# Kernel optimization log

Hardware: AMD Instinct MI355X
Metric: run time of the kernel (lower is better)

The kernel has to match this reference:

```python
import jax, jax.numpy as jnp
import numpy as np

B = 512
D_MODEL = 512
D_STATE = 128
D_CONV = 2
EXPAND = 2
D_INNER = EXPAND * D_MODEL          # 1024
DT_RANK = (D_MODEL + 15) // 16      # 32 (mamba default 'auto')
HIDDEN = 256


def setup_inputs() -> dict:
    key = jax.random.key(0)
    ks = jax.random.split(key, 12)
    s = 0.02
    f32 = jnp.float32
    inp = {
        "x": jax.random.normal(ks[0], (B, D_MODEL), f32),
        # Mamba params (torch Linear weight layout: [out, in])
        "in_proj_w": jax.random.normal(ks[1], (2 * D_INNER, D_MODEL), f32) * s,
        "conv_w": jax.random.normal(ks[2], (D_INNER, D_CONV), f32) * s,  # depthwise kernel
        "conv_b": jnp.zeros((D_INNER,), f32),
        "x_proj_w": jax.random.normal(ks[3], (DT_RANK + 2 * D_STATE, D_INNER), f32) * s,
        "dt_proj_w": jax.random.normal(ks[4], (D_INNER, DT_RANK), f32) * s,
        "dt_proj_b": jax.random.normal(ks[5], (D_INNER,), f32) * s,
        "A_log": jnp.log(jnp.broadcast_to(
            jnp.arange(1, D_STATE + 1, dtype=f32), (D_INNER, D_STATE)).copy()),
        "D": jnp.ones((D_INNER,), f32),
        "out_proj_w": jax.random.normal(ks[6], (D_MODEL, D_INNER), f32) * s,
        # head params
        "fc1_w": jax.random.normal(ks[7], (HIDDEN, D_MODEL), f32) * s,
        "fc1_b": jnp.zeros((HIDDEN,), f32),
        "fc5_w": jax.random.normal(ks[8], (1, HIDDEN), f32) * s,
        "fc5_b": jnp.zeros((1,), f32),
    }
    return inp


def _mamba(x3, in_proj_w, conv_w, conv_b, x_proj_w, dt_proj_w, dt_proj_b,
           A_log, D, out_proj_w):
    # x3: [B, L, d_model]
    Bn, L, _ = x3.shape
    xz = jnp.einsum('bld,ed->ble', x3, in_proj_w)          # [B, L, 2*d_inner]
    xin, z = xz[..., :D_INNER], xz[..., D_INNER:]
    # depthwise causal conv1d (kernel D_CONV, padding D_CONV-1, truncated to L)
    xp = jnp.pad(xin, ((0, 0), (D_CONV - 1, 0), (0, 0)))
    conv = conv_b
    for k in range(D_CONV):
        conv = conv + conv_w[:, k] * xp[:, k:k + L, :]
    xin = jax.nn.silu(conv)                                 # [B, L, d_inner]
    x_dbl = jnp.einsum('blc,ec->ble', xin, x_proj_w)        # [B, L, dt_rank+2*d_state]
    dt = x_dbl[..., :DT_RANK]
    Bm = x_dbl[..., DT_RANK:DT_RANK + D_STATE]              # [B, L, d_state]
    Cm = x_dbl[..., DT_RANK + D_STATE:]                     # [B, L, d_state]
    dt = jax.nn.softplus(jnp.einsum('blr,cr->blc', dt, dt_proj_w) + dt_proj_b)
    A = -jnp.exp(A_log)                                     # [d_inner, d_state]
    dA = jnp.exp(dt[..., None] * A)                         # [B, L, d_inner, d_state]
    dBu = dt[..., None] * Bm[:, :, None, :] * xin[..., None]

    def step(h, t):
        dA_t, dBu_t, C_t = t
        h = dA_t * h + dBu_t                                # [B, d_inner, d_state]
        y_t = jnp.einsum('bcs,bs->bc', h, C_t)
        return h, y_t

    h0 = jnp.zeros((Bn, D_INNER, D_STATE), x3.dtype)
    _, ys = jax.lax.scan(step, h0, (dA.transpose(1, 0, 2, 3),
                                    dBu.transpose(1, 0, 2, 3),
                                    Cm.transpose(1, 0, 2)))
    y = ys.transpose(1, 0, 2)                               # [B, L, d_inner]
    y = (y + D * xin) * jax.nn.silu(z)
    return jnp.einsum('blc,dc->bld', y, out_proj_w)         # [B, L, d_model]


def reference(x, in_proj_w, conv_w, conv_b, x_proj_w, dt_proj_w, dt_proj_b,
              A_log, D, out_proj_w, fc1_w, fc1_b, fc5_w, fc5_b):
    h = _mamba(x[:, None, :], in_proj_w, conv_w, conv_b, x_proj_w,
               dt_proj_w, dt_proj_b, A_log, D, out_proj_w)[:, 0, :]
    h = h @ fc1_w.T + fc1_b
    h = jnp.where(h >= 0, h, 0.1 * h)   # LeakyReLU(0.1); dropout is eval-mode identity
    h = h @ fc5_w.T + fc5_b
    return jax.nn.sigmoid(h)            # [B, 1]
```

## Files before the change

kernel.cpp:

```cpp
#include <hip/hip_runtime.h>
#include <hip/hip_bf16.h>
#include <cstddef>

typedef __attribute__((ext_vector_type(8))) short short8;
typedef __attribute__((ext_vector_type(4))) float f32x4;

#define MFMA16(a, b, c) __builtin_amdgcn_mfma_f32_16x16x32_bf16((a), (b), (c), 0, 0, 0)

static __device__ __forceinline__ unsigned short f2bf(float f) {
    unsigned int u = __float_as_uint(f);
    u = (u + 0x7FFFu + ((u >> 16) & 1u)) >> 16;
    return (unsigned short)u;
}
static __device__ __forceinline__ float bf2f(unsigned short h) {
    return __uint_as_float(((unsigned int)h) << 16);
}
static __device__ __forceinline__ float silu_f(float v) { return v / (1.f + expf(-v)); }

static __device__ __forceinline__ short8 cvt_frag(const float* __restrict__ p) {
    float4 a = *reinterpret_cast<const float4*>(p);
    float4 b = *reinterpret_cast<const float4*>(p + 4);
    union { short8 s; unsigned int u[4]; } r;
    asm("v_cvt_pk_bf16_f32 %0, %1, %2" : "=v"(r.u[0]) : "v"(a.x), "v"(a.y));
    asm("v_cvt_pk_bf16_f32 %0, %1, %2" : "=v"(r.u[1]) : "v"(a.z), "v"(a.w));
    asm("v_cvt_pk_bf16_f32 %0, %1, %2" : "=v"(r.u[2]) : "v"(b.x), "v"(b.y));
    asm("v_cvt_pk_bf16_f32 %0, %1, %2" : "=v"(r.u[3]) : "v"(b.z), "v"(b.w));
    return r.s;
}

enum : size_t {
    O_X     = 0,
    O_WIP   = O_X    + 512 * 512,
    O_WXP   = O_WIP  + 2048 * 512,
    O_WDT   = O_WXP  + 288 * 1024,
    O_WOUT  = O_WDT  + 1024 * 32,
    O_WFC1  = O_WOUT + 512 * 1024,
    O_XIN   = O_WFC1 + 256 * 512,
    O_SZ    = O_XIN  + 512 * 1024,
    O_Y     = O_SZ   + 512 * 1024,
    O_F32   = O_Y    + 512 * 1024,
};
#define N_XDBLF (512 * 288)
#define N_MOUTF (512 * 512)
#define N_ZERO  (N_XDBLF + N_MOUTF)

static __device__ __forceinline__ void cvt_seg(const float* __restrict__ s,
                                               unsigned short* __restrict__ d,
                                               int n, int gt, int np)
{
    for (int i = gt * 4; i < n; i += np * 4) {
        float4 v = *reinterpret_cast<const float4*>(s + i);
        ushort4 o;
        o.x = f2bf(v.x); o.y = f2bf(v.y); o.z = f2bf(v.z); o.w = f2bf(v.w);
        *reinterpret_cast<ushort4*>(d + i) = o;
    }
}

__global__ __launch_bounds__(256) void k_convert(
    const float* __restrict__ x,    const float* __restrict__ wip,
    const float* __restrict__ wxp,  const float* __restrict__ wdt,
    const float* __restrict__ wout, const float* __restrict__ wfc1,
    unsigned short* __restrict__ wsb)
{
    const int gt = blockIdx.x * blockDim.x + threadIdx.x;
    const int np = gridDim.x * blockDim.x;
    cvt_seg(x,    wsb + O_X,    512 * 512,  gt, np);
    cvt_seg(wip,  wsb + O_WIP,  2048 * 512, gt, np);
    cvt_seg(wxp,  wsb + O_WXP,  288 * 1024, gt, np);
    cvt_seg(wdt,  wsb + O_WDT,  1024 * 32,  gt, np);
    cvt_seg(wout, wsb + O_WOUT, 512 * 1024, gt, np);
    cvt_seg(wfc1, wsb + O_WFC1, 256 * 512,  gt, np);
    float* z = (float*)(wsb + O_F32);
    const float4 z4 = make_float4(0.f, 0.f, 0.f, 0.f);
    for (int i = gt * 4; i < N_ZERO; i += np * 4)
        *reinterpret_cast<float4*>(z + i) = z4;
}

__global__ __launch_bounds__(256, 4) void k_s1(
    unsigned short* __restrict__ wsb,
    const float* __restrict__ cw, const float* __restrict__ cb)
{
    const int tid = threadIdx.x;
    const int w = tid >> 6, lane = tid & 63, l15 = lane & 15, g = lane >> 4;
    const int n0 = blockIdx.x * 64 + w * 16;
    const int m0 = blockIdx.y * 16;

    const unsigned short* arow = wsb + O_X   + (size_t)(m0 + l15) * 512 + g * 8;
    const unsigned short* brow = wsb + O_WIP + (size_t)(n0 + l15) * 512 + g * 8;

    f32x4 acc = {};
#pragma unroll 4
    for (int k0 = 0; k0 < 512; k0 += 32) {
        short8 a = *reinterpret_cast<const short8*>(arow + k0);
        short8 b = *reinterpret_cast<const short8*>(brow + k0);
        acc = MFMA16(a, b, acc);
    }
    const bool xhalf = (blockIdx.x < 16);
    unsigned short* dst = wsb + (xhalf ? O_XIN : O_SZ);
    int n = n0 + l15;
    int c = xhalf ? n : n - 1024;
    float cwv = 0.f, cbv = 0.f;
    if (xhalf) { cwv = cw[2 * n + 1]; cbv = cb[n]; }
#pragma unroll
    for (int i = 0; i < 4; ++i) {
        float v = acc[i];
        v = xhalf ? silu_f(cbv + cwv * v) : silu_f(v);
        dst[(size_t)(m0 + g * 4 + i) * 1024 + c] = f2bf(v);
    }
}

__global__ __launch_bounds__(256, 4) void k_s2(
    unsigned short* __restrict__ wsb, float* __restrict__ xdblf)
{
    const int tid = threadIdx.x;
    const int w = tid >> 6, lane = tid & 63, l15 = lane & 15, g = lane >> 4;
    const int n0 = blockIdx.x * 16;
    const int m0 = blockIdx.y * 64 + w * 16;
    const int kq = blockIdx.z * 256;

    const unsigned short* arow = wsb + O_XIN + (size_t)(m0 + l15) * 1024 + kq + g * 8;
    const unsigned short* brow = wsb + O_WXP + (size_t)(n0 + l15) * 1024 + kq + g * 8;

    f32x4 acc = {};
#pragma unroll 4
    for (int k0 = 0; k0 < 256; k0 += 32) {
        short8 a = *reinterpret_cast<const short8*>(arow + k0);
        short8 b = *reinterpret_cast<const short8*>(brow + k0);
        acc = MFMA16(a, b, acc);
    }
#pragma unroll
    for (int i = 0; i < 4; ++i)
        atomicAdd(&xdblf[(size_t)(m0 + g * 4 + i) * 288 + n0 + l15], acc[i]);
}

__global__ __launch_bounds__(256, 4) void k_s3(
    unsigned short* __restrict__ wsb, const float* __restrict__ xdblf,
    const float* __restrict__ dtb, const float* __restrict__ Dv)
{
    __shared__ float bcp[16][17];
    __shared__ float bc_s[16];
    const int tid = threadIdx.x;
    const int w = tid >> 6, lane = tid & 63, l15 = lane & 15, g = lane >> 4;
    const int n0 = blockIdx.x * 64;
    const int m0 = blockIdx.y * 16;

    {
        int r = tid >> 4, p = tid & 15;
        const float* row = xdblf + (size_t)(m0 + r) * 288;
        float s = 0.f;
#pragma unroll
        for (int q = 0; q < 8; ++q)
            s += row[32 + p * 8 + q] * row[160 + p * 8 + q];
        bcp[r][p] = s;
    }
    short8 a3 = cvt_frag(xdblf + (size_t)(m0 + l15) * 288 + g * 8);
    __syncthreads();
    if (tid < 16) {
        float s = 0.f;
#pragma unroll
        for (int p = 0; p < 16; ++p) s += bcp[tid][p];
        bc_s[tid] = s;
    }
    __syncthreads();

    const unsigned short* xinb = wsb + O_XIN;
    const unsigned short* szb  = wsb + O_SZ;
    unsigned short* yb = wsb + O_Y;
    const f32x4 z4 = {0.f, 0.f, 0.f, 0.f};
    int n = n0 + w * 16 + l15;
    short8 b = *reinterpret_cast<const short8*>(wsb + O_WDT + (size_t)n * 32 + g * 8);
    f32x4 acc = MFMA16(a3, b, z4);
    float dtbv = dtb[n], Dvv = Dv[n];
#pragma unroll
    for (int i = 0; i < 4; ++i) {
        int r = m0 + g * 4 + i;
        float dtv = acc[i] + dtbv;
        dtv = (dtv > 20.f) ? dtv : log1pf(expf(dtv));
        float yv = bf2f(xinb[(size_t)r * 1024 + n]) *
                   (dtv * bc_s[g * 4 + i] + Dvv) *
                   bf2f(szb[(size_t)r * 1024 + n]);
        yb[(size_t)r * 1024 + n] = f2bf(yv);
    }
}

__global__ __launch_bounds__(256, 4) void k_s4(
    unsigned short* __restrict__ wsb, float* __restrict__ moutf)
{
    const int tid = threadIdx.x;
    const int w = tid >> 6, lane = tid & 63, l15 = lane & 15, g = lane >> 4;
    const int n0 = blockIdx.x * 64 + w * 16;
    const int m0 = blockIdx.y * 16;
    const int kq = blockIdx.z * 512;

    const unsigned short* arow = wsb + O_Y    + (size_t)(m0 + l15) * 1024 + kq + g * 8;
    const unsigned short* brow = wsb + O_WOUT + (size_t)(n0 + l15) * 1024 + kq + g * 8;

    f32x4 acc = {};
#pragma unroll 4
    for (int k0 = 0; k0 < 512; k0 += 32) {
        short8 a = *reinterpret_cast<const short8*>(arow + k0);
        short8 b = *reinterpret_cast<const short8*>(brow + k0);
        acc = MFMA16(a, b, acc);
    }
#pragma unroll
    for (int i = 0; i < 4; ++i)
        atomicAdd(&moutf[(size_t)(m0 + g * 4 + i) * 512 + n0 + l15], acc[i]);
}

__global__ __launch_bounds__(512, 2) void k_s5(
    const float* __restrict__ moutf, unsigned short* __restrict__ wsb,
    const float* __restrict__ bfc1, const float* __restrict__ wfc5,
    const float* __restrict__ bfc5, float* __restrict__ out)
{
    __shared__ float red[16][8];
    const int tid = threadIdx.x;
    const int w = tid >> 6, lane = tid & 63, l15 = lane & 15, g = lane >> 4;
    const int m0 = blockIdx.x * 16;

    const float* arow = moutf + (size_t)(m0 + l15) * 512 + g * 8;
    const unsigned short* brow = wsb + O_WFC1 + (size_t)(w * 32 + l15) * 512 + g * 8;

    f32x4 acc[2] = {};
#pragma unroll 4
    for (int k0 = 0; k0 < 512; k0 += 32) {
        short8 a = cvt_frag(arow + k0);
#pragma unroll
        for (int f = 0; f < 2; ++f) {
            short8 b = *reinterpret_cast<const short8*>(brow + (size_t)f * 16 * 512 + k0);
            acc[f] = MFMA16(a, b, acc[f]);
        }
    }
    float part[4] = {0.f, 0.f, 0.f, 0.f};
#pragma unroll
    for (int f = 0; f < 2; ++f) {
        int n = w * 32 + f * 16 + l15;
        float b1 = bfc1[n], w5 = wfc5[n];
#pragma unroll
        for (int i = 0; i < 4; ++i) {
            float v = acc[f][i] + b1;
            v = v >= 0.f ? v : 0.1f * v;
            part[i] = fmaf(v, w5, part[i]);
        }
    }
#pragma unroll
    for (int off = 1; off < 16; off <<= 1)
#pragma unroll
        for (int i = 0; i < 4; ++i) part[i] += __shfl_xor(part[i], off, 64);
    if (l15 == 0)
#pragma unroll
        for (int i = 0; i < 4; ++i) red[g * 4 + i][w] = part[i];
    __syncthreads();
    if (tid < 16) {
        float s = 0.f;
#pragma unroll
        for (int j = 0; j < 8; ++j) s += red[tid][j];
        out[m0 + tid] = 1.f / (1.f + expf(-(s + bfc5[0])));
    }
}

extern "C" void kernel_launch(void* const* d_in, const int* in_sizes, int n_in,
                              void* d_out, int out_size, void* d_ws, size_t ws_size,
                              hipStream_t stream)
{
    const float* x    = (const float*)d_in[0];
    const float* wip  = (const float*)d_in[1];
    const float* cw   = (const float*)d_in[2];
    const float* cb   = (const float*)d_in[3];
    const float* wxp  = (const float*)d_in[4];
    const float* wdt  = (const float*)d_in[5];
    const float* bdt  = (const float*)d_in[6];
    const float* Dv   = (const float*)d_in[8];
    const float* wout = (const float*)d_in[9];
    const float* wfc1 = (const float*)d_in[10];
    const float* bfc1 = (const float*)d_in[11];
    const float* wfc5 = (const float*)d_in[12];
    const float* bfc5 = (const float*)d_in[13];
    float* out = (float*)d_out;

    unsigned short* wsb = (unsigned short*)d_ws;
    float* xdblf = (float*)(wsb + O_F32);
    float* moutf = xdblf + N_XDBLF;

    k_convert<<<dim3(1024),    256, 0, stream>>>(x, wip, wxp, wdt, wout, wfc1, wsb);
    k_s1     <<<dim3(32, 32),  256, 0, stream>>>(wsb, cw, cb);
    k_s2     <<<dim3(18, 8, 4),256, 0, stream>>>(wsb, xdblf);
    k_s3     <<<dim3(16, 32),  256, 0, stream>>>(wsb, xdblf, bdt, Dv);
    k_s4     <<<dim3(8, 32, 2),256, 0, stream>>>(wsb, moutf);
    k_s5     <<<dim3(32),      512, 0, stream>>>(moutf, wsb, bfc1, wfc5, bfc5, out);
}
```

Measured before the change: 142.2 us.

## Fold out_proj into fc1 weights and fuse final two GEMM stages

Uses associativity to precompute W45 = fc1_w @ out_proj_w (256x1024) inside the prep kernel via an LDS-transposed MFMA, then computes the head GEMM directly from y against W45. This removes the out_proj GEMM kernel, its atomicAdd reduction, the moutf zeroing, and one launch. The cost is an extra weight-product GEMM each call inside prep (256 of the blocks do it) and slightly different bf16 rounding, since the product is rounded once rather than the intermediate activations.

Measured after the change: 149.5 us. 5.1% more time.

```diff
diff --git a/kernel.cpp b/kernel.cpp
--- a/kernel.cpp
+++ b/kernel.cpp
@@ -33,16 +33,13 @@
     O_WIP   = O_X    + 512 * 512,
     O_WXP   = O_WIP  + 2048 * 512,
     O_WDT   = O_WXP  + 288 * 1024,
-    O_WOUT  = O_WDT  + 1024 * 32,
-    O_WFC1  = O_WOUT + 512 * 1024,
-    O_XIN   = O_WFC1 + 256 * 512,
+    O_W45   = O_WDT  + 1024 * 32,
+    O_XIN   = O_W45  + 256 * 1024,
     O_SZ    = O_XIN  + 512 * 1024,
     O_Y     = O_SZ   + 512 * 1024,
     O_F32   = O_Y    + 512 * 1024,
 };
 #define N_XDBLF (512 * 288)
-#define N_MOUTF (512 * 512)
-#define N_ZERO  (N_XDBLF + N_MOUTF)
 
 static __device__ __forceinline__ void cvt_seg(const float* __restrict__ s,
                                                unsigned short* __restrict__ d,
@@ -56,24 +53,49 @@
     }
 }
 
-__global__ __launch_bounds__(256) void k_convert(
+__global__ __launch_bounds__(256) void k_prep(
     const float* __restrict__ x,    const float* __restrict__ wip,
     const float* __restrict__ wxp,  const float* __restrict__ wdt,
     const float* __restrict__ wout, const float* __restrict__ wfc1,
     unsigned short* __restrict__ wsb)
 {
-    const int gt = blockIdx.x * blockDim.x + threadIdx.x;
-    const int np = gridDim.x * blockDim.x;
-    cvt_seg(x,    wsb + O_X,    512 * 512,  gt, np);
-    cvt_seg(wip,  wsb + O_WIP,  2048 * 512, gt, np);
-    cvt_seg(wxp,  wsb + O_WXP,  288 * 1024, gt, np);
-    cvt_seg(wdt,  wsb + O_WDT,  1024 * 32,  gt, np);
-    cvt_seg(wout, wsb + O_WOUT, 512 * 1024, gt, np);
-    cvt_seg(wfc1, wsb + O_WFC1, 256 * 512,  gt, np);
-    float* z = (float*)(wsb + O_F32);
-    const float4 z4 = make_float4(0.f, 0.f, 0.f, 0.f);
-    for (int i = gt * 4; i < N_ZERO; i += np * 4)
-        *reinterpret_cast<float4*>(z + i) = z4;
+    const int tid = threadIdx.x;
+    const int bid = blockIdx.x;
+    {
+        const int gt = bid * 256 + tid, np = 1024 * 256;
+        cvt_seg(x,   wsb + O_X,   512 * 512,  gt, np);
+        cvt_seg(wip, wsb + O_WIP, 2048 * 512, gt, np);
+        cvt_seg(wxp, wsb + O_WXP, 288 * 1024, gt, np);
+        cvt_seg(wdt, wsb + O_WDT, 1024 * 32,  gt, np);
+        float* z = (float*)(wsb + O_F32);
+        const float4 z4 = make_float4(0.f, 0.f, 0.f, 0.f);
+        for (int i = gt * 4; i < N_XDBLF; i += np * 4)
+            *reinterpret_cast<float4*>(z + i) = z4;
+    }
+    if (bid < 256) {
+        __shared__ __align__(16) float t[64][36];
+        const int w = tid >> 6, lane = tid & 63, l15 = lane & 15, g = lane >> 4;
+        const int j0 = (bid >> 4) * 16;
+        const int c0 = (bid & 15) * 64;
+        f32x4 acc = {};
+        for (int d0 = 0; d0 < 512; d0 += 32) {
+            int r = tid >> 3, cc = (tid & 7) * 8;
+            float4 v0 = *reinterpret_cast<const float4*>(wout + (size_t)(d0 + r) * 1024 + c0 + cc);
+            float4 v1 = *reinterpret_cast<const float4*>(wout + (size_t)(d0 + r) * 1024 + c0 + cc + 4);
+            t[cc + 0][r] = v0.x; t[cc + 1][r] = v0.y; t[cc + 2][r] = v0.z; t[cc + 3][r] = v0.w;
+            t[cc + 4][r] = v1.x; t[cc + 5][r] = v1.y; t[cc + 6][r] = v1.z; t[cc + 7][r] = v1.w;
+            __syncthreads();
+            short8 a = cvt_frag(wfc1 + (size_t)(j0 + l15) * 512 + d0 + g * 8);
+            short8 b = cvt_frag(&t[w * 16 + l15][g * 8]);
+            acc = MFMA16(a, b, acc);
+            __syncthreads();
+        }
+        unsigned short* w45 = wsb + O_W45;
+        int c = c0 + w * 16 + l15;
+#pragma unroll
+        for (int i = 0; i < 4; ++i)
+            w45[(size_t)(j0 + g * 4 + i) * 1024 + c] = f2bf(acc[i]);
+    }
 }
 
 __global__ __launch_bounds__(256, 4) void k_s1(
@@ -183,32 +205,8 @@
     }
 }
 
-__global__ __launch_bounds__(256, 4) void k_s4(
-    unsigned short* __restrict__ wsb, float* __restrict__ moutf)
-{
-    const int tid = threadIdx.x;
-    const int w = tid >> 6, lane = tid & 63, l15 = lane & 15, g = lane >> 4;
-    const int n0 = blockIdx.x * 64 + w * 16;
-    const int m0 = blockIdx.y * 16;
-    const int kq = blockIdx.z * 512;
-
-    const unsigned short* arow = wsb + O_Y    + (size_t)(m0 + l15) * 1024 + kq + g * 8;
-    const unsigned short* brow = wsb + O_WOUT + (size_t)(n0 + l15) * 1024 + kq + g * 8;
-
-    f32x4 acc = {};
-#pragma unroll 4
-    for (int k0 = 0; k0 < 512; k0 += 32) {
-        short8 a = *reinterpret_cast<const short8*>(arow + k0);
-        short8 b = *reinterpret_cast<const short8*>(brow + k0);
-        acc = MFMA16(a, b, acc);
-    }
-#pragma unroll
-    for (int i = 0; i < 4; ++i)
-        atomicAdd(&moutf[(size_t)(m0 + g * 4 + i) * 512 + n0 + l15], acc[i]);
-}
-
-__global__ __launch_bounds__(512, 2) void k_s5(
-    const float* __restrict__ moutf, unsigned short* __restrict__ wsb,
+__global__ __launch_bounds__(512, 2) void k_s45(
+    unsigned short* __restrict__ wsb,
     const float* __restrict__ bfc1, const float* __restrict__ wfc5,
     const float* __restrict__ bfc5, float* __restrict__ out)
 {
@@ -217,16 +215,16 @@
     const int w = tid >> 6, lane = tid & 63, l15 = lane & 15, g = lane >> 4;
     const int m0 = blockIdx.x * 16;
 
-    const float* arow = moutf + (size_t)(m0 + l15) * 512 + g * 8;
-    const unsigned short* brow = wsb + O_WFC1 + (size_t)(w * 32 + l15) * 512 + g * 8;
+    const unsigned short* arow = wsb + O_Y   + (size_t)(m0 + l15) * 1024 + g * 8;
+    const unsigned short* brow = wsb + O_W45 + (size_t)(w * 32 + l15) * 1024 + g * 8;
 
     f32x4 acc[2] = {};
 #pragma unroll 4
-    for (int k0 = 0; k0 < 512; k0 += 32) {
-        short8 a = cvt_frag(arow + k0);
+    for (int k0 = 0; k0 < 1024; k0 += 32) {
+        short8 a = *reinterpret_cast<const short8*>(arow + k0);
 #pragma unroll
         for (int f = 0; f < 2; ++f) {
-            short8 b = *reinterpret_cast<const short8*>(brow + (size_t)f * 16 * 512 + k0);
+            short8 b = *reinterpret_cast<const short8*>(brow + (size_t)f * 16 * 1024 + k0);
             acc[f] = MFMA16(a, b, acc[f]);
         }
     }
@@ -279,12 +277,10 @@
 
     unsigned short* wsb = (unsigned short*)d_ws;
     float* xdblf = (float*)(wsb + O_F32);
-    float* moutf = xdblf + N_XDBLF;
-
-    k_convert<<<dim3(1024),    256, 0, stream>>>(x, wip, wxp, wdt, wout, wfc1, wsb);
-    k_s1     <<<dim3(32, 32),  256, 0, stream>>>(wsb, cw, cb);
-    k_s2     <<<dim3(18, 8, 4),256, 0, stream>>>(wsb, xdblf);
-    k_s3     <<<dim3(16, 32),  256, 0, stream>>>(wsb, xdblf, bdt, Dv);
-    k_s4     <<<dim3(8, 32, 2),256, 0, stream>>>(wsb, moutf);
-    k_s5     <<<dim3(32),      512, 0, stream>>>(moutf, wsb, bfc1, wfc5, bfc5, out);
-}
+
+    k_prep<<<dim3(1024),    256, 0, stream>>>(x, wip, wxp, wdt, wout, wfc1, wsb);
+    k_s1  <<<dim3(32, 32),  256, 0, stream>>>(wsb, cw, cb);
+    k_s2  <<<dim3(18, 8, 4),256, 0, stream>>>(wsb, xdblf);
+    k_s3  <<<dim3(16, 32),  256, 0, stream>>>(wsb, xdblf, bdt, Dv);
+    k_s45 <<<dim3(32),      512, 0, stream>>>(wsb, bfc1, wfc5, bfc5, out);
+}
```
